# Optimization experiments

Hardware: AMD Instinct MI355X
Metric: run time of the kernel (lower is better)

## Reference

```python
import jax, jax.numpy as jnp
import numpy as np

DIM = 256
NUM_HEADS = 8
HEAD_DIM = DIM // NUM_HEADS


def setup_inputs() -> dict:
    key = jax.random.key(0)
    k_x, k_wq, k_bq, k_wp, k_bp = jax.random.split(key, 5)
    x = jax.random.normal(k_x, (4, DIM, 64, 64), dtype=jnp.float32)
    # 1x1 convs == per-pixel linear layers over channels
    w_qkv = jax.random.normal(k_wq, (3 * DIM, DIM), dtype=jnp.float32) * (DIM ** -0.5)
    b_qkv = jax.random.normal(k_bq, (3 * DIM,), dtype=jnp.float32) * 0.02
    w_proj = jax.random.normal(k_wp, (DIM, DIM), dtype=jnp.float32) * (DIM ** -0.5)
    b_proj = jax.random.normal(k_bp, (DIM,), dtype=jnp.float32) * 0.02
    return {"x": x, "w_qkv": w_qkv, "b_qkv": b_qkv, "w_proj": w_proj, "b_proj": b_proj}


def reference(x, w_qkv, b_qkv, w_proj, b_proj):
    B, C, H, W = x.shape
    S = H * W
    h, d = NUM_HEADS, HEAD_DIM
    # flatten spatial dims: (B, C, H, W) -> (B, S, C)
    xf = x.reshape(B, C, S).transpose(0, 2, 1)
    # 1x1 conv qkv: (B, S, 3C)
    qkv = xf @ w_qkv.T + b_qkv
    q, k, v = jnp.split(qkv, 3, axis=-1)
    # channel dim splits as (heads, head_dim): (B, S, C) -> (B, h, S, d)
    split = lambda t: t.reshape(B, S, h, d).transpose(0, 2, 1, 3)
    q, k, v = split(q), split(k), split(v)
    scale = d ** -0.5
    attn = jnp.einsum('bhsd,bhtd->bhst', q, k) * scale  # (B, h, S, S)
    attn = jax.nn.softmax(attn, axis=-1)
    out = jnp.einsum('bhst,bhtd->bhsd', attn, v)
    # merge heads: (B, h, S, d) -> (B, S, C)
    out = out.transpose(0, 2, 1, 3).reshape(B, S, C)
    out = out @ w_proj.T + b_proj
    # back to (B, C, H, W)
    return out.transpose(0, 2, 1).reshape(B, C, H, W)
```

## Files before the change

### kernel.cpp

```cpp
#include <hip/hip_runtime.h>


typedef __attribute__((ext_vector_type(8))) short short8;
typedef __attribute__((ext_vector_type(4))) float f4;

__device__ __forceinline__ short f2bs(float f) {
  union { float f; unsigned u; } v; v.f = f;
  unsigned r = v.u + 0x7FFFu + ((v.u >> 16) & 1u);
  return (short)(r >> 16);
}

__device__ __forceinline__ short8 cvt8(f4 a, f4 b) {
  short8 o;
  o[0] = f2bs(a[0]); o[1] = f2bs(a[1]); o[2] = f2bs(a[2]); o[3] = f2bs(a[3]);
  o[4] = f2bs(b[0]); o[5] = f2bs(b[1]); o[6] = f2bs(b[2]); o[7] = f2bs(b[3]);
  return o;
}

#if __has_builtin(__builtin_amdgcn_cvt_pk_bf16_f32)
__device__ __forceinline__ int pk2(float a, float b) {
  auto v = __builtin_amdgcn_cvt_pk_bf16_f32(a, b);
  int r;
  __builtin_memcpy(&r, &v, 4);
  return r;
}
#else
__device__ __forceinline__ int pk2(float a, float b) {
  return (int)((unsigned short)f2bs(a) | ((unsigned)f2bs(b) << 16));
}
#endif

__global__ __launch_bounds__(256) void k_qkv(
    const float* __restrict__ x, const float* __restrict__ w,
    const float* __restrict__ bias,
    short* __restrict__ Qr, short* __restrict__ Kq, short* __restrict__ Vt) {
  const int tid = threadIdx.x;
  const int L = tid & 63, wv = tid >> 6;
  const int ln15 = L & 15, quad = L >> 4;
  const int mt = blockIdx.x;
  const int b = mt >> 6;
  const int s0 = (mt & 63) << 6;
  const int j0 = blockIdx.y << 6;
  const int jw = j0 + wv * 16;

  __shared__ __align__(16) short tl[4 * 64 * 16];

  f4 acc[4] = {{0,0,0,0},{0,0,0,0},{0,0,0,0},{0,0,0,0}};
  const float* wb = w + (jw + ln15) * 256 + quad * 8;
  const float* xb = x + b * (256 * 4096) + s0 + ln15;

#pragma unroll 2
  for (int cb = 0; cb < 256; cb += 32) {
    f4 a0 = *(const f4*)(wb + cb);
    f4 a1 = *(const f4*)(wb + cb + 4);
    short8 af = cvt8(a0, a1);
    const float* xc = xb + (cb + quad * 8) * 4096;
#pragma unroll
    for (int sub = 0; sub < 4; ++sub) {
      const float* xs = xc + sub * 16;
      short8 bf;
#pragma unroll
      for (int jj = 0; jj < 8; ++jj) bf[jj] = f2bs(xs[jj * 4096]);
      acc[sub] = __builtin_amdgcn_mfma_f32_16x16x32_bf16(af, bf, acc[sub], 0, 0, 0);
    }
  }

  float bj[4];
#pragma unroll
  for (int r = 0; r < 4; ++r) bj[r] = bias[jw + quad * 4 + r];

  const int type = j0 >> 8;
  if (type == 2) {
    const int jv = jw - 512;
    const int h = jv >> 5;
    const int dbase = jv & 31;
#pragma unroll
    for (int r = 0; r < 4; ++r) {
      const int d = dbase + quad * 4 + r;
      short* vp = Vt + (size_t)((b * 8 + h) * 32 + d) * 4096 + s0 + ln15;
#pragma unroll
      for (int sub = 0; sub < 4; ++sub)
        vp[sub * 16] = f2bs(acc[sub][r] + bj[r]);
    }
  } else {
    const float qsc = 0.17677669529663689f * 1.44269504088896f;
    const float mul = (type == 0) ? qsc : 1.0f;
    short* dst = (type == 0) ? Qr : Kq;
    const int hj = jw & 255;
    short* tw = tl + wv * 1024;
#pragma unroll
    for (int sub = 0; sub < 4; ++sub) {
      const int s = sub * 16 + ln15;
      const int swz = (s >> 2) & 1;
#pragma unroll
      for (int r = 0; r < 4; ++r) {
        const int dl = quad * 4 + r;
        tw[s * 16 + (((dl >> 3) ^ swz) * 8) + (dl & 7)] = f2bs((acc[sub][r] + bj[r]) * mul);
      }
    }
    const int h = hj >> 5;
    const int d0 = hj & 31;
#pragma unroll
    for (int i = 0; i < 2; ++i) {
      const int sl = i * 32 + (L >> 1);
      const int gg = L & 1;
      const int g2 = gg ^ ((sl >> 2) & 1);
      short8 row = *(const short8*)(tw + sl * 16 + g2 * 8);
      *(short8*)(dst + (size_t)((b * 8 + h) * 4096 + s0 + sl) * 32 + d0 + gg * 8) = row;
    }
  }
}

__global__ __launch_bounds__(256) void k_attn(
    const short* __restrict__ Qr, const short* __restrict__ Kq,
    const short* __restrict__ Vt, short* __restrict__ O) {
  const int tid = threadIdx.x;
  const int L = tid & 63, wv = tid >> 6;
  const int ln15 = L & 15, quad = L >> 4;
  const int bh = blockIdx.y;
  const int b = bh >> 3, h = bh & 7;
  const int qb = blockIdx.x * 128 + wv * 32;

  const short* Qb = Qr + (size_t)bh * 4096 * 32;
  const short* Kb = Kq + (size_t)bh * 4096 * 32;
  const short* Vb = Vt + (size_t)bh * 32 * 4096;

  __shared__ __align__(16) short plds[4 * 2048];
  short* pw = plds + wv * 2048;
  const int swz = (ln15 & 7) << 1;

  short8 qf[2];
#pragma unroll
  for (int qs = 0; qs < 2; ++qs)
    qf[qs] = *(const short8*)(Qb + (qb + qs * 16 + ln15) * 32 + quad * 8);

  f4 acc[2][2] = {{{0,0,0,0},{0,0,0,0}},{{0,0,0,0},{0,0,0,0}}};
  float lsum[2] = {0.f, 0.f};

  const short* kp = Kb + ln15 * 32 + quad * 8;
  const short* vp = Vb + ln15 * 4096 + quad * 8;

#pragma unroll 2
  for (int kb = 0; kb < 4096; kb += 64) {
#pragma unroll
    for (int t = 0; t < 4; ++t) {
      short8 kf = *(const short8*)(kp + (kb + t * 16) * 32);
#pragma unroll
      for (int qs = 0; qs < 2; ++qs) {
        f4 z = {0.f, 0.f, 0.f, 0.f};
        f4 sc = __builtin_amdgcn_mfma_f32_16x16x32_bf16(kf, qf[qs], z, 0, 0, 0);
        float p0 = __builtin_amdgcn_exp2f(sc[0]);
        float p1 = __builtin_amdgcn_exp2f(sc[1]);
        float p2 = __builtin_amdgcn_exp2f(sc[2]);
        float p3 = __builtin_amdgcn_exp2f(sc[3]);
        lsum[qs] += (p0 + p1) + (p2 + p3);
        int2 pr;
        pr.x = pk2(p0, p1);
        pr.y = pk2(p2, p3);
        const int g = (4 * t + quad) ^ swz;
        *(int2*)(pw + qs * 1024 + ln15 * 64 + g * 4) = pr;
      }
    }
#pragma unroll
    for (int ks = 0; ks < 2; ++ks) {
      short8 pf[2];
#pragma unroll
      for (int qs = 0; qs < 2; ++qs) {
        const int g0 = (8 * ks + 2 * quad) ^ swz;
        pf[qs] = *(const short8*)(pw + qs * 1024 + ln15 * 64 + g0 * 4);
      }
#pragma unroll
      for (int dg = 0; dg < 2; ++dg) {
        short8 vf = *(const short8*)(vp + dg * (16 * 4096) + kb + ks * 32);
        acc[0][dg] = __builtin_amdgcn_mfma_f32_16x16x32_bf16(pf[0], vf, acc[0][dg], 0, 0, 0);
        acc[1][dg] = __builtin_amdgcn_mfma_f32_16x16x32_bf16(pf[1], vf, acc[1][dg], 0, 0, 0);
      }
    }
  }

#pragma unroll
  for (int qs = 0; qs < 2; ++qs) {
    float l = lsum[qs];
    l += __shfl_xor(l, 16);
    l += __shfl_xor(l, 32);
    const float rl = 1.0f / l;
#pragma unroll
    for (int r = 0; r < 4; ++r) {
      const float rlr = __shfl(rl, quad * 4 + r);
      const int sg = qb + qs * 16 + quad * 4 + r;
      short* op = O + (size_t)(b * 4096 + sg) * 256 + h * 32 + ln15;
      op[0]  = f2bs(acc[qs][0][r] * rlr);
      op[16] = f2bs(acc[qs][1][r] * rlr);
    }
  }
}

__global__ __launch_bounds__(256) void k_proj(
    const short* __restrict__ O, const float* __restrict__ w,
    const float* __restrict__ bias, float* __restrict__ out) {
  const int tid = threadIdx.x;
  const int L = tid & 63, wv = tid >> 6;
  const int ln15 = L & 15, quad = L >> 4;
  const int m0 = blockIdx.x * 64 + wv * 16;
  const int n0 = blockIdx.y << 6;
  const int b = m0 >> 12, s0 = m0 & 4095;

  f4 acc[4] = {{0,0,0,0},{0,0,0,0},{0,0,0,0},{0,0,0,0}};
  const short* Ob = O + (size_t)(m0 + ln15) * 256 + quad * 8;
  const float* wb = w + (n0 + ln15) * 256 + quad * 8;

#pragma unroll 2
  for (int cb = 0; cb < 256; cb += 32) {
    short8 af = *(const short8*)(Ob + cb);
#pragma unroll
    for (int sub = 0; sub < 4; ++sub) {
      f4 b0 = *(const f4*)(wb + sub * (16 * 256) + cb);
      f4 b1 = *(const f4*)(wb + sub * (16 * 256) + cb + 4);
      short8 bf = cvt8(b0, b1);
      acc[sub] = __builtin_amdgcn_mfma_f32_16x16x32_bf16(af, bf, acc[sub], 0, 0, 0);
    }
  }

  __shared__ float tl[4][64 * 17];
  float* tw = tl[wv];
#pragma unroll
  for (int sub = 0; sub < 4; ++sub) {
    const float bv = bias[n0 + sub * 16 + ln15];
#pragma unroll
    for (int r = 0; r < 4; ++r)
      tw[(sub * 16 + ln15) * 17 + quad * 4 + r] = acc[sub][r] + bv;
  }
#pragma unroll
  for (int i = 0; i < 4; ++i) {
    const int c = i * 16 + (L >> 2);
    const int ms = (L & 3) * 4;
    f4 v;
#pragma unroll
    for (int j = 0; j < 4; ++j) v[j] = tw[c * 17 + ms + j];
    *(f4*)(out + (size_t)b * (256 * 4096) + (size_t)(n0 + c) * 4096 + s0 + ms) = v;
  }
}

extern "C" void kernel_launch(void* const* d_in, const int* in_sizes, int n_in,
                              void* d_out, int out_size, void* d_ws, size_t ws_size,
                              hipStream_t stream) {
  const float* x      = (const float*)d_in[0];
  const float* w_qkv  = (const float*)d_in[1];
  const float* b_qkv  = (const float*)d_in[2];
  const float* w_proj = (const float*)d_in[3];
  const float* b_proj = (const float*)d_in[4];
  float* out = (float*)d_out;

  const size_t SEG = (size_t)4 * 8 * 4096 * 32;
  short* Qr = (short*)d_ws;
  short* Kq = Qr + SEG;
  short* Vt = Kq + SEG;
  short* O  = Vt + SEG;

  k_qkv <<<dim3(256, 12), 256, 0, stream>>>(x, w_qkv, b_qkv, Qr, Kq, Vt);
  k_attn<<<dim3(32, 32),  256, 0, stream>>>(Qr, Kq, Vt, O);
  k_proj<<<dim3(256, 4),  256, 0, stream>>>(O, w_proj, b_proj, out);
}
```

Baseline: 352.8 us.

## Split attention keys across wave pairs and compute row sums via MFMA

The attention kernel now splits the 4096 keys into two halves handled by different waves of the same block. The partial outputs and row sums are combined through shared memory at the end, and the grid is doubled to 64x32 blocks. The per-row softmax denominator comes from an extra MFMA against a ones vector instead of scalar adds and shuffles. The fp32-to-bf16 packing of probabilities now uses a byte-permute truncation instead of round-to-nearest conversion. This raises parallelism and cuts VALU work, at the cost of one more MFMA per tile, a block-wide sync, a final shared-memory reduction, and slightly less accurate rounding.

```diff
diff --git a/kernel.cpp b/kernel.cpp
--- a/kernel.cpp
+++ b/kernel.cpp
@@ -17,18 +17,10 @@
   return o;
 }
 
-#if __has_builtin(__builtin_amdgcn_cvt_pk_bf16_f32)
-__device__ __forceinline__ int pk2(float a, float b) {
-  auto v = __builtin_amdgcn_cvt_pk_bf16_f32(a, b);
-  int r;
-  __builtin_memcpy(&r, &v, 4);
-  return r;
-}
-#else
-__device__ __forceinline__ int pk2(float a, float b) {
-  return (int)((unsigned short)f2bs(a) | ((unsigned)f2bs(b) << 16));
-}
-#endif
+__device__ __forceinline__ int pktrunc(float lo, float hi) {
+  union { float f; unsigned u; } a, b; a.f = lo; b.f = hi;
+  return (int)__builtin_amdgcn_perm(b.u, a.u, 0x07060302u);
+}
 
 __global__ __launch_bounds__(256) void k_qkv(
     const float* __restrict__ x, const float* __restrict__ w,
@@ -119,78 +111,101 @@
   const int ln15 = L & 15, quad = L >> 4;
   const int bh = blockIdx.y;
   const int b = bh >> 3, h = bh & 7;
-  const int qb = blockIdx.x * 128 + wv * 32;
+  const int qt = wv & 1, half = wv >> 1;
+  const int qb = blockIdx.x * 64 + qt * 32;
 
   const short* Qb = Qr + (size_t)bh * 4096 * 32;
-  const short* Kb = Kq + (size_t)bh * 4096 * 32;
-  const short* Vb = Vt + (size_t)bh * 32 * 4096;
-
-  __shared__ __align__(16) short plds[4 * 2048];
-  short* pw = plds + wv * 2048;
-  const int swz = (ln15 & 7) << 1;
+  const short* Kb = Kq + (size_t)bh * 4096 * 32 + half * 2048 * 32;
+  const short* Vb = Vt + (size_t)bh * 32 * 4096 + half * 2048;
+
+  __shared__ __align__(16) short plds[4][2048];
+  __shared__ float l_up[2][32];
+  short* pw = plds[wv];
+  const int sw = ln15 & 14;
 
   short8 qf[2];
 #pragma unroll
   for (int qs = 0; qs < 2; ++qs)
     qf[qs] = *(const short8*)(Qb + (qb + qs * 16 + ln15) * 32 + quad * 8);
 
+  short8 onef = {0, 0, 0, 0, 0, 0, 0, 0};
+  if (ln15 == 0) {
+#pragma unroll
+    for (int j = 0; j < 8; ++j) onef[j] = (short)0x3F80;
+  }
+
   f4 acc[2][2] = {{{0,0,0,0},{0,0,0,0}},{{0,0,0,0},{0,0,0,0}}};
-  float lsum[2] = {0.f, 0.f};
+  f4 accl[2] = {{0,0,0,0},{0,0,0,0}};
+  const f4 z4 = {0.f, 0.f, 0.f, 0.f};
 
   const short* kp = Kb + ln15 * 32 + quad * 8;
   const short* vp = Vb + ln15 * 4096 + quad * 8;
 
-#pragma unroll 2
-  for (int kb = 0; kb < 4096; kb += 64) {
+  for (int kb = 0; kb < 2048; kb += 64) {
 #pragma unroll
     for (int t = 0; t < 4; ++t) {
       short8 kf = *(const short8*)(kp + (kb + t * 16) * 32);
 #pragma unroll
       for (int qs = 0; qs < 2; ++qs) {
-        f4 z = {0.f, 0.f, 0.f, 0.f};
-        f4 sc = __builtin_amdgcn_mfma_f32_16x16x32_bf16(kf, qf[qs], z, 0, 0, 0);
+        f4 sc = __builtin_amdgcn_mfma_f32_16x16x32_bf16(kf, qf[qs], z4, 0, 0, 0);
         float p0 = __builtin_amdgcn_exp2f(sc[0]);
         float p1 = __builtin_amdgcn_exp2f(sc[1]);
         float p2 = __builtin_amdgcn_exp2f(sc[2]);
         float p3 = __builtin_amdgcn_exp2f(sc[3]);
-        lsum[qs] += (p0 + p1) + (p2 + p3);
         int2 pr;
-        pr.x = pk2(p0, p1);
-        pr.y = pk2(p2, p3);
-        const int g = (4 * t + quad) ^ swz;
-        *(int2*)(pw + qs * 1024 + ln15 * 64 + g * 4) = pr;
+        pr.x = pktrunc(p0, p1);
+        pr.y = pktrunc(p2, p3);
+        const int gw = ((t << 2) + quad) ^ sw;
+        *(int2*)(pw + qs * 1024 + ln15 * 64 + gw * 4) = pr;
       }
     }
 #pragma unroll
     for (int ks = 0; ks < 2; ++ks) {
-      short8 pf[2];
+      short8 vf0 = *(const short8*)(vp + kb + ks * 32);
+      short8 vf1 = *(const short8*)(vp + 16 * 4096 + kb + ks * 32);
 #pragma unroll
       for (int qs = 0; qs < 2; ++qs) {
-        const int g0 = (8 * ks + 2 * quad) ^ swz;
-        pf[qs] = *(const short8*)(pw + qs * 1024 + ln15 * 64 + g0 * 4);
-      }
-#pragma unroll
-      for (int dg = 0; dg < 2; ++dg) {
-        short8 vf = *(const short8*)(vp + dg * (16 * 4096) + kb + ks * 32);
-        acc[0][dg] = __builtin_amdgcn_mfma_f32_16x16x32_bf16(pf[0], vf, acc[0][dg], 0, 0, 0);
-        acc[1][dg] = __builtin_amdgcn_mfma_f32_16x16x32_bf16(pf[1], vf, acc[1][dg], 0, 0, 0);
-      }
-    }
-  }
-
-#pragma unroll
-  for (int qs = 0; qs < 2; ++qs) {
-    float l = lsum[qs];
-    l += __shfl_xor(l, 16);
-    l += __shfl_xor(l, 32);
-    const float rl = 1.0f / l;
-#pragma unroll
-    for (int r = 0; r < 4; ++r) {
-      const float rlr = __shfl(rl, quad * 4 + r);
-      const int sg = qb + qs * 16 + quad * 4 + r;
-      short* op = O + (size_t)(b * 4096 + sg) * 256 + h * 32 + ln15;
-      op[0]  = f2bs(acc[qs][0][r] * rlr);
-      op[16] = f2bs(acc[qs][1][r] * rlr);
+        const int g0 = ((ks << 3) + (quad << 1)) ^ sw;
+        short8 pf = *(const short8*)(pw + qs * 1024 + ln15 * 64 + g0 * 4);
+        acc[qs][0] = __builtin_amdgcn_mfma_f32_16x16x32_bf16(pf, vf0, acc[qs][0], 0, 0, 0);
+        acc[qs][1] = __builtin_amdgcn_mfma_f32_16x16x32_bf16(pf, vf1, acc[qs][1], 0, 0, 0);
+        accl[qs]   = __builtin_amdgcn_mfma_f32_16x16x32_bf16(pf, onef, accl[qs], 0, 0, 0);
+      }
+    }
+  }
+
+  if (half == 1) {
+    float* cw = (float*)plds[wv];
+#pragma unroll
+    for (int qs = 0; qs < 2; ++qs) {
+#pragma unroll
+      for (int dg = 0; dg < 2; ++dg)
+#pragma unroll
+        for (int r = 0; r < 4; ++r)
+          cw[(qs * 16 + quad * 4 + r) * 32 + dg * 16 + ln15] = acc[qs][dg][r];
+      if (ln15 == 0) {
+#pragma unroll
+        for (int r = 0; r < 4; ++r)
+          l_up[qt][qs * 16 + quad * 4 + r] = accl[qs][r];
+      }
+    }
+  }
+  __syncthreads();
+  if (half == 0) {
+    const float* cu = (const float*)plds[wv + 2];
+#pragma unroll
+    for (int qs = 0; qs < 2; ++qs) {
+#pragma unroll
+      for (int r = 0; r < 4; ++r) {
+        const float lown = __shfl(accl[qs][r], quad << 4);
+        const float lup = l_up[qt][qs * 16 + quad * 4 + r];
+        const float rl = 1.0f / (lown + lup);
+        const int sg = qb + qs * 16 + quad * 4 + r;
+        short* op = O + (size_t)(b * 4096 + sg) * 256 + h * 32 + ln15;
+        const int ci = (qs * 16 + quad * 4 + r) * 32 + ln15;
+        op[0]  = f2bs((acc[qs][0][r] + cu[ci]) * rl);
+        op[16] = f2bs((acc[qs][1][r] + cu[ci + 16]) * rl);
+      }
     }
   }
 }
@@ -258,6 +273,6 @@
   short* O  = Vt + SEG;
 
   k_qkv <<<dim3(256, 12), 256, 0, stream>>>(x, w_qkv, b_qkv, Qr, Kq, Vt);
-  k_attn<<<dim3(32, 32),  256, 0, stream>>>(Qr, Kq, Vt, O);
+  k_attn<<<dim3(64, 32),  256, 0, stream>>>(Qr, Kq, Vt, O);
   k_proj<<<dim3(256, 4),  256, 0, stream>>>(O, w_proj, b_proj, out);
 }
```

Measured after the change: 337.3 us. -4.4%, faster.
